# Optimization experiments

Hardware: AMD Instinct MI355X
Metric: run time of the kernel (lower is better)

Reference implementation:

```python
import jax, jax.numpy as jnp
import numpy as np

TOP_K = 2


def setup_inputs() -> dict:
    key = jax.random.key(0)
    ks = jax.random.split(key, 6)
    B, S, D, F, E = 4, 2048, 1024, 4096, 8
    sd = 1.0 / np.sqrt(D)
    sf = 1.0 / np.sqrt(F)
    return {
        "x": jax.random.normal(ks[0], (B, S, D), dtype=jnp.float32),
        "gate_w": jax.random.normal(ks[1], (D, E), dtype=jnp.float32) * sd,
        "w1": jax.random.normal(ks[2], (E, D, F), dtype=jnp.float32) * sd,
        "b1": jax.random.normal(ks[3], (E, F), dtype=jnp.float32) * 0.01,
        "w2": jax.random.normal(ks[4], (E, F, D), dtype=jnp.float32) * sf,
        "b2": jax.random.normal(ks[5], (E, D), dtype=jnp.float32) * 0.01,
    }


def reference(x, gate_w, w1, b1, w2, b2):
    B, S, D = x.shape
    E = gate_w.shape[1]
    xf = x.reshape(-1, D)                        # [T, D], T = B*S
    T = xf.shape[0]

    # Gating: top-k logits, softmax over the selected k (in fp32, as in torch)
    logits = xf @ gate_w                         # [T, E]
    top_vals, top_idx = jax.lax.top_k(logits, TOP_K)            # [T, K]
    wts = jax.nn.softmax(top_vals.astype(jnp.float32), axis=-1).astype(x.dtype)

    # Dense combine weights: combine[t, e] = sum_k wts[t,k] * [top_idx[t,k]==e]
    rows = jnp.arange(T)[:, None]
    combine = jnp.zeros((T, E), dtype=x.dtype).at[rows, top_idx].add(wts)

    # Expert FFNs (dropout is identity in eval; torch GELU default = exact erf)
    out = jnp.zeros_like(xf)
    for e in range(E):
        h = jax.nn.gelu(xf @ w1[e] + b1[e], approximate=False)  # [T, F]
        out = out + combine[:, e:e + 1] * (h @ w2[e] + b2[e])
    return out.reshape(B, S, D)
```

## Files before the change

### kernel.cpp

```cpp
#include <hip/hip_runtime.h>


#define T_TOK 8192
#define D_DIM 1024
#define F_DIM 4096
#define E_NUM 8
#define BM 256
#define BN 256
#define BK 64
#define NK1 (D_DIM / BK)
#define NK2 (F_DIM / BK)
#define NX1 (F_DIM / BN)
#define NX2 (D_DIM / BN)
#define MAX_TILES (T_TOK * 2 / BM + E_NUM)

typedef float f32x4 __attribute__((ext_vector_type(4)));
typedef short bf16x8 __attribute__((ext_vector_type(8)));

__device__ __forceinline__ unsigned short f2bf(float f) {
  union { float f; unsigned u; } v; v.f = f;
  unsigned r = v.u + 0x7FFFu + ((v.u >> 16) & 1u);
  return (unsigned short)(r >> 16);
}

__device__ __forceinline__ void async_cp16(const unsigned short* g, unsigned short* l) {
  __builtin_amdgcn_global_load_lds((__attribute__((address_space(1))) void*)g,
                                   (__attribute__((address_space(3))) void*)l,
                                   16, 0, 0);
}

#define WAIT_VM6 asm volatile("s_waitcnt vmcnt(6)" ::: "memory")
#define WAIT_LGKM0 asm volatile("s_waitcnt lgkmcnt(0)" ::: "memory")
#define RAW_BARRIER asm volatile("s_barrier" ::: "memory")


__global__ void cast_x_kernel(const float* __restrict__ src,
                              unsigned short* __restrict__ dst, int n4) {
  int i = blockIdx.x * blockDim.x + threadIdx.x;
  if (i >= n4) return;
  float4 v = ((const float4*)src)[i];
  ushort4 o;
  o.x = f2bf(v.x); o.y = f2bf(v.y); o.z = f2bf(v.z); o.w = f2bf(v.w);
  ((ushort4*)dst)[i] = o;
}

__global__ __launch_bounds__(256) void transpose_cast_kernel(
    const float* __restrict__ src, unsigned short* __restrict__ dst,
    int R, int C) {
  __shared__ float tile[64][65];
  int e = blockIdx.z;
  src += (size_t)e * R * C;
  dst += (size_t)e * R * C;
  int c0 = blockIdx.x * 64;
  int r0 = blockIdx.y * 64;
  int t = threadIdx.x;
  int cl = (t & 15) * 4, rl = t >> 4;
#pragma unroll
  for (int i = 0; i < 4; ++i) {
    int r = rl + i * 16;
    float4 v = *(const float4*)(src + (size_t)(r0 + r) * C + c0 + cl);
    tile[r][cl + 0] = v.x;
    tile[r][cl + 1] = v.y;
    tile[r][cl + 2] = v.z;
    tile[r][cl + 3] = v.w;
  }
  __syncthreads();
  int rl2 = (t & 15) * 4, cl2 = t >> 4;
#pragma unroll
  for (int i = 0; i < 4; ++i) {
    int c = cl2 + i * 16;
    ushort4 o;
    o.x = f2bf(tile[rl2 + 0][c]);
    o.y = f2bf(tile[rl2 + 1][c]);
    o.z = f2bf(tile[rl2 + 2][c]);
    o.w = f2bf(tile[rl2 + 3][c]);
    *(ushort4*)(dst + (size_t)(c0 + c) * R + r0 + rl2) = o;
  }
}

__global__ __launch_bounds__(256) void gate_kernel(
    const float* __restrict__ x, const float* __restrict__ gw,
    float* __restrict__ topk_w, int* __restrict__ topk_e) {
  int t = (blockIdx.x * 256 + threadIdx.x) >> 6;
  int lane = threadIdx.x & 63;
  const float* xr = x + (size_t)t * D_DIM;
  float acc[8];
#pragma unroll
  for (int e = 0; e < 8; ++e) acc[e] = 0.f;
  for (int j = 0; j < D_DIM / 64; ++j) {
    int d = lane + 64 * j;
    float xv = xr[d];
    float4 g0 = ((const float4*)(gw + (size_t)d * 8))[0];
    float4 g1 = ((const float4*)(gw + (size_t)d * 8))[1];
    acc[0] += xv * g0.x; acc[1] += xv * g0.y;
    acc[2] += xv * g0.z; acc[3] += xv * g0.w;
    acc[4] += xv * g1.x; acc[5] += xv * g1.y;
    acc[6] += xv * g1.z; acc[7] += xv * g1.w;
  }
#pragma unroll
  for (int off = 32; off > 0; off >>= 1) {
#pragma unroll
    for (int e = 0; e < 8; ++e) acc[e] += __shfl_xor(acc[e], off);
  }
  if (lane == 0) {
    int e0 = 0; float v0 = acc[0];
#pragma unroll
    for (int e = 1; e < 8; ++e)
      if (acc[e] > v0) { v0 = acc[e]; e0 = e; }
    int e1 = -1; float v1 = -1e30f;
#pragma unroll
    for (int e = 0; e < 8; ++e)
      if (e != e0 && acc[e] > v1) { v1 = acc[e]; e1 = e; }
    float ex = expf(v1 - v0);
    float inv = 1.f / (1.f + ex);
    topk_w[2 * t] = inv;
    topk_w[2 * t + 1] = ex * inv;
    topk_e[2 * t] = e0;
    topk_e[2 * t + 1] = e1;
  }
}

__global__ void scatter_kernel(const int* __restrict__ topk_e,
                               int* __restrict__ cnt, int* __restrict__ assign) {
  int idx = blockIdx.x * blockDim.x + threadIdx.x;
  int e = topk_e[idx];
  int pos = atomicAdd(&cnt[e], 1);
  assign[e * T_TOK + pos] = idx;
}

__global__ void tiles_kernel(const int* __restrict__ cnt,
                             int* __restrict__ ndesc, int4* __restrict__ desc) {
  if (threadIdx.x != 0) return;
  int nt = 0, hb = 0;
  for (int e = 0; e < E_NUM; ++e) {
    int c = cnt[e];
    for (int s = 0; s < c; s += BM) {
      int4 d;
      d.x = e; d.y = s; d.z = hb;
      d.w = (c - s < BM) ? (c - s) : BM;
      desc[nt++] = d;
    }
    hb += c;
  }
  *ndesc = nt;
}


__global__ __launch_bounds__(512, 2) void gemm1_kernel(
    const unsigned short* __restrict__ xb, const unsigned short* __restrict__ w1t,
    const float* __restrict__ b1, const int* __restrict__ assign,
    const int* __restrict__ ndesc, const int4* __restrict__ desc,
    unsigned short* __restrict__ H) {
  const int nwg = NX1 * MAX_TILES;
  int lin = blockIdx.y * NX1 + blockIdx.x;
  int wg = (lin & 7) * (nwg >> 3) + (lin >> 3);
  int tileid = wg / NX1;
  int n0 = (wg & (NX1 - 1)) * BN;
  if (tileid >= *ndesc) return;
  int4 dc = desc[tileid];
  int e = dc.x, start = dc.y, hbase = dc.z, mcnt = dc.w;

  extern __shared__ __attribute__((aligned(16))) unsigned short smem[];

  int tid = threadIdx.x, lane = tid & 63, wv = tid >> 6;

  int drow = tid >> 3, dcc = tid & 7;
  int g = (dcc - drow) & 7;
  const unsigned short* gAr[4];
  const unsigned short* gBr[4];
#pragma unroll
  for (int j = 0; j < 4; ++j) {
    int r = drow + 64 * j;
    int rc = r < mcnt ? r : (mcnt - 1);
    int a = assign[e * T_TOK + start + rc];
    gAr[j] = xb + (size_t)(a >> 1) * D_DIM + g * 8;
    gBr[j] = w1t + (size_t)(e * F_DIM + n0 + r) * D_DIM + g * 8;
  }
  int ldst = wv * 512;

  int kc16 = lane >> 4, r16 = lane & 15;
  int m_off = (wv & 1) * 128, n_off = (wv >> 1) * 64;

  f32x4 acc[8][4];
#pragma unroll
  for (int i = 0; i < 8; ++i)
#pragma unroll
    for (int j = 0; j < 4; ++j) acc[i][j] = (f32x4){0.f, 0.f, 0.f, 0.f};
  bf16x8 bfr[4][2];

  auto issueA = [&](int t, int j) {
    int kt = t < NK1 ? t : NK1 - 1;
    async_cp16(gAr[j] + kt * 64, smem + (t & 1) * 32768 + ldst + j * 4096);
  };
  auto issueB = [&](int t, int j) {
    int kt = t < NK1 ? t : NK1 - 1;
    async_cp16(gBr[j] + kt * 64, smem + (t & 1) * 32768 + 16384 + ldst + j * 4096);
  };

  auto phase = [&](int t, int q) {
    const unsigned short* Ab = smem + (t & 1) * 32768;
    const unsigned short* Bb = Ab + 16384;
    if (q == 0) {
#pragma unroll
      for (int j = 0; j < 4; ++j) {
        int rb = n_off + j * 16 + r16;
#pragma unroll
        for (int h = 0; h < 2; ++h)
          bfr[j][h] = *(const bf16x8*)(Bb + rb * 64 + ((h * 4 + kc16 + rb) & 7) * 8);
      }
    }
    bf16x8 af[2][2];
#pragma unroll
    for (int m2 = 0; m2 < 2; ++m2) {
      int ra = m_off + (2 * q + m2) * 16 + r16;
#pragma unroll
      for (int h = 0; h < 2; ++h)
        af[m2][h] = *(const bf16x8*)(Ab + ra * 64 + ((h * 4 + kc16 + ra) & 7) * 8);
    }
    if (q == 0)      { issueA(t + 1, 1); issueA(t + 1, 3); }
    else if (q == 1) { issueB(t + 2, 0); issueB(t + 2, 1); }
    else if (q == 2) { issueB(t + 2, 2); issueB(t + 2, 3); }
    else             { issueA(t + 2, 0); issueA(t + 2, 2); }
    RAW_BARRIER;
    WAIT_LGKM0;
    __builtin_amdgcn_s_setprio(1);
#pragma unroll
    for (int h = 0; h < 2; ++h)
#pragma unroll
      for (int m2 = 0; m2 < 2; ++m2)
#pragma unroll
        for (int j = 0; j < 4; ++j)
          acc[2 * q + m2][j] = __builtin_amdgcn_mfma_f32_16x16x32_bf16(
              af[m2][h], bfr[j][h], acc[2 * q + m2][j], 0, 0, 0);
    __builtin_amdgcn_s_setprio(0);
    if (q == 3) WAIT_VM6;
    RAW_BARRIER;
  };

#pragma unroll
  for (int j = 0; j < 4; ++j) issueB(0, j);
#pragma unroll
  for (int j = 0; j < 4; ++j) issueA(0, j);
  issueB(1, 0); issueB(1, 1); issueB(1, 2); issueB(1, 3);
  issueA(1, 0); issueA(1, 2);
  WAIT_VM6;
  RAW_BARRIER;

  for (int t = 0; t < NK1; ++t) {
    phase(t, 0); phase(t, 1); phase(t, 2); phase(t, 3);
  }

  int col = lane & 15, rbase = (lane >> 4) * 4;
  float bias[4];
#pragma unroll
  for (int j = 0; j < 4; ++j) bias[j] = b1[e * F_DIM + n0 + n_off + j * 16 + col];
#pragma unroll
  for (int i = 0; i < 8; ++i) {
#pragma unroll
    for (int rg = 0; rg < 4; ++rg) {
      int r = m_off + i * 16 + rbase + rg;
      if (r < mcnt) {
        unsigned short* hrow = H + (size_t)(hbase + start + r) * F_DIM + n0 + n_off + col;
#pragma unroll
        for (int j = 0; j < 4; ++j) {
          float v = acc[i][j][rg] + bias[j];
          v = 0.5f * v * (1.0f + erff(v * 0.70710678118654752f));
          hrow[j * 16] = f2bf(v);
        }
      }
    }
  }
}

__global__ __launch_bounds__(512, 2) void gemm2_kernel(
    const unsigned short* __restrict__ H, const unsigned short* __restrict__ w2t,
    const float* __restrict__ b2, const int* __restrict__ assign,
    const float* __restrict__ topk_w,
    const int* __restrict__ ndesc, const int4* __restrict__ desc,
    float* __restrict__ out) {
  const int nwg = NX2 * MAX_TILES;
  int lin = blockIdx.y * NX2 + blockIdx.x;
  int wg = (lin & 7) * (nwg >> 3) + (lin >> 3);
  int tileid = wg / NX2;
  int n0 = (wg & (NX2 - 1)) * BN;
  if (tileid >= *ndesc) return;
  int4 dc = desc[tileid];
  int e = dc.x, start = dc.y, hbase = dc.z, mcnt = dc.w;

  extern __shared__ __attribute__((aligned(16))) unsigned short smem[];

  int tid = threadIdx.x, lane = tid & 63, wv = tid >> 6;

  int drow = tid >> 3, dcc = tid & 7;
  int g = (dcc - drow) & 7;
  const unsigned short* gAr[4];
  const unsigned short* gBr[4];
#pragma unroll
  for (int j = 0; j < 4; ++j) {
    int r = drow + 64 * j;
    int rc = r < mcnt ? r : (mcnt - 1);
    gAr[j] = H + (size_t)(hbase + start + rc) * F_DIM + g * 8;
    gBr[j] = w2t + (size_t)(e * D_DIM + n0 + r) * F_DIM + g * 8;
  }
  int ldst = wv * 512;

  int kc16 = lane >> 4, r16 = lane & 15;
  int m_off = (wv & 1) * 128, n_off = (wv >> 1) * 64;

  f32x4 acc[8][4];
#pragma unroll
  for (int i = 0; i < 8; ++i)
#pragma unroll
    for (int j = 0; j < 4; ++j) acc[i][j] = (f32x4){0.f, 0.f, 0.f, 0.f};
  bf16x8 bfr[4][2];

  auto issueA = [&](int t, int j) {
    int kt = t < NK2 ? t : NK2 - 1;
    async_cp16(gAr[j] + kt * 64, smem + (t & 1) * 32768 + ldst + j * 4096);
  };
  auto issueB = [&](int t, int j) {
    int kt = t < NK2 ? t : NK2 - 1;
    async_cp16(gBr[j] + kt * 64, smem + (t & 1) * 32768 + 16384 + ldst + j * 4096);
  };

  auto phase = [&](int t, int q) {
    const unsigned short* Ab = smem + (t & 1) * 32768;
    const unsigned short* Bb = Ab + 16384;
    if (q == 0) {
#pragma unroll
      for (int j = 0; j < 4; ++j) {
        int rb = n_off + j * 16 + r16;
#pragma unroll
        for (int h = 0; h < 2; ++h)
          bfr[j][h] = *(const bf16x8*)(Bb + rb * 64 + ((h * 4 + kc16 + rb) & 7) * 8);
      }
    }
    bf16x8 af[2][2];
#pragma unroll
    for (int m2 = 0; m2 < 2; ++m2) {
      int ra = m_off + (2 * q + m2) * 16 + r16;
#pragma unroll
      for (int h = 0; h < 2; ++h)
        af[m2][h] = *(const bf16x8*)(Ab + ra * 64 + ((h * 4 + kc16 + ra) & 7) * 8);
    }
    if (q == 0)      { issueA(t + 1, 1); issueA(t + 1, 3); }
    else if (q == 1) { issueB(t + 2, 0); issueB(t + 2, 1); }
    else if (q == 2) { issueB(t + 2, 2); issueB(t + 2, 3); }
    else             { issueA(t + 2, 0); issueA(t + 2, 2); }
    RAW_BARRIER;
    WAIT_LGKM0;
    __builtin_amdgcn_s_setprio(1);
#pragma unroll
    for (int h = 0; h < 2; ++h)
#pragma unroll
      for (int m2 = 0; m2 < 2; ++m2)
#pragma unroll
        for (int j = 0; j < 4; ++j)
          acc[2 * q + m2][j] = __builtin_amdgcn_mfma_f32_16x16x32_bf16(
              af[m2][h], bfr[j][h], acc[2 * q + m2][j], 0, 0, 0);
    __builtin_amdgcn_s_setprio(0);
    if (q == 3) WAIT_VM6;
    RAW_BARRIER;
  };

#pragma unroll
  for (int j = 0; j < 4; ++j) issueB(0, j);
#pragma unroll
  for (int j = 0; j < 4; ++j) issueA(0, j);
  issueB(1, 0); issueB(1, 1); issueB(1, 2); issueB(1, 3);
  issueA(1, 0); issueA(1, 2);
  WAIT_VM6;
  RAW_BARRIER;

  for (int t = 0; t < NK2; ++t) {
    phase(t, 0); phase(t, 1); phase(t, 2); phase(t, 3);
  }

  int col = lane & 15, rbase = (lane >> 4) * 4;
  float bias[4];
#pragma unroll
  for (int j = 0; j < 4; ++j) bias[j] = b2[e * D_DIM + n0 + n_off + j * 16 + col];
#pragma unroll
  for (int i = 0; i < 8; ++i) {
#pragma unroll
    for (int rg = 0; rg < 4; ++rg) {
      int r = m_off + i * 16 + rbase + rg;
      if (r < mcnt) {
        int a = assign[e * T_TOK + start + r];
        float wt = topk_w[a];
        float* orow = out + (size_t)(a >> 1) * D_DIM + n0 + n_off + col;
#pragma unroll
        for (int j = 0; j < 4; ++j) {
          float v = acc[i][j][rg] + bias[j];
          atomicAdd(orow + j * 16, wt * v);
        }
      }
    }
  }
}


extern "C" void kernel_launch(void* const* d_in, const int* in_sizes, int n_in,
                              void* d_out, int out_size, void* d_ws, size_t ws_size,
                              hipStream_t stream) {
  const float* x      = (const float*)d_in[0];
  const float* gate_w = (const float*)d_in[1];
  const float* w1     = (const float*)d_in[2];
  const float* b1     = (const float*)d_in[3];
  const float* w2     = (const float*)d_in[4];
  const float* b2     = (const float*)d_in[5];
  float* out = (float*)d_out;

  char* ws = (char*)d_ws;
  size_t off = 0;
  auto alloc = [&](size_t bytes) {
    char* p = ws + off;
    off = (off + bytes + 255) & ~(size_t)255;
    return p;
  };
  unsigned short* xb   = (unsigned short*)alloc((size_t)T_TOK * D_DIM * 2);
  unsigned short* w1t  = (unsigned short*)alloc((size_t)E_NUM * D_DIM * F_DIM * 2);
  unsigned short* w2t  = (unsigned short*)alloc((size_t)E_NUM * D_DIM * F_DIM * 2);
  unsigned short* Hbuf = (unsigned short*)alloc((size_t)2 * T_TOK * F_DIM * 2);
  float* topk_w = (float*)alloc((size_t)2 * T_TOK * 4);
  int* topk_e   = (int*)alloc((size_t)2 * T_TOK * 4);
  int* assign   = (int*)alloc((size_t)E_NUM * T_TOK * 4);
  int* cnt      = (int*)alloc(64);
  int* ndesc    = (int*)alloc(64);
  int4* desc    = (int4*)alloc((size_t)MAX_TILES * 16);

  hipFuncSetAttribute(reinterpret_cast<const void*>(gemm1_kernel),
                      hipFuncAttributeMaxDynamicSharedMemorySize, 131072);
  hipFuncSetAttribute(reinterpret_cast<const void*>(gemm2_kernel),
                      hipFuncAttributeMaxDynamicSharedMemorySize, 131072);

  hipMemsetAsync(cnt, 0, 64, stream);
  hipMemsetAsync(out, 0, (size_t)out_size * 4, stream);

  cast_x_kernel<<<(T_TOK * D_DIM / 4 + 255) / 256, 256, 0, stream>>>(
      x, xb, T_TOK * D_DIM / 4);
  transpose_cast_kernel<<<dim3(F_DIM / 64, D_DIM / 64, E_NUM), 256, 0, stream>>>(
      w1, w1t, D_DIM, F_DIM);
  transpose_cast_kernel<<<dim3(D_DIM / 64, F_DIM / 64, E_NUM), 256, 0, stream>>>(
      w2, w2t, F_DIM, D_DIM);
  gate_kernel<<<T_TOK / 4, 256, 0, stream>>>(x, gate_w, topk_w, topk_e);
  scatter_kernel<<<2 * T_TOK / 256, 256, 0, stream>>>(topk_e, cnt, assign);
  tiles_kernel<<<1, 64, 0, stream>>>(cnt, ndesc, desc);
  gemm1_kernel<<<dim3(NX1, MAX_TILES), 512, 131072, stream>>>(
      xb, w1t, b1, assign, ndesc, desc, Hbuf);
  gemm2_kernel<<<dim3(NX2, MAX_TILES), 512, 131072, stream>>>(
      Hbuf, w2t, b2, assign, topk_w, ndesc, desc, out);
}
```

Before: 935.1 us.

## Shrink gemm2 M-tile, fuse x cast into gate, aggregate scatter atomics

The x-to-bf16 cast moves into the gate kernel, removing a separate pass. The transpose-cast kernel now writes wider 16-byte stores. Scatter uses wave-level ballot aggregation, so there is one atomic per expert per wave. gemm2 gets its own 128-row tile descriptors, with smaller LDS use and a two-phase pipeline to increase workgroup count and occupancy for the narrow N=1024 GEMM. One barrier is also dropped in gemm1's phase loop, which risks an LDS race if the remaining synchronization is insufficient.

```diff
diff --git a/kernel.cpp b/kernel.cpp
--- a/kernel.cpp
+++ b/kernel.cpp
@@ -13,9 +13,12 @@
 #define NX1 (F_DIM / BN)
 #define NX2 (D_DIM / BN)
 #define MAX_TILES (T_TOK * 2 / BM + E_NUM)
+#define BM2 128
+#define MAX_TILES2 (T_TOK * 2 / BM2 + E_NUM)
 
 typedef float f32x4 __attribute__((ext_vector_type(4)));
 typedef short bf16x8 __attribute__((ext_vector_type(8)));
+typedef unsigned short u16x8 __attribute__((ext_vector_type(8)));
 
 __device__ __forceinline__ unsigned short f2bf(float f) {
   union { float f; unsigned u; } v; v.f = f;
@@ -30,19 +33,10 @@
 }
 
 #define WAIT_VM6 asm volatile("s_waitcnt vmcnt(6)" ::: "memory")
+#define WAIT_VM4 asm volatile("s_waitcnt vmcnt(4)" ::: "memory")
 #define WAIT_LGKM0 asm volatile("s_waitcnt lgkmcnt(0)" ::: "memory")
 #define RAW_BARRIER asm volatile("s_barrier" ::: "memory")
 
-
-__global__ void cast_x_kernel(const float* __restrict__ src,
-                              unsigned short* __restrict__ dst, int n4) {
-  int i = blockIdx.x * blockDim.x + threadIdx.x;
-  if (i >= n4) return;
-  float4 v = ((const float4*)src)[i];
-  ushort4 o;
-  o.x = f2bf(v.x); o.y = f2bf(v.y); o.z = f2bf(v.z); o.w = f2bf(v.w);
-  ((ushort4*)dst)[i] = o;
-}
 
 __global__ __launch_bounds__(256) void transpose_cast_kernel(
     const float* __restrict__ src, unsigned short* __restrict__ dst,
@@ -65,31 +59,32 @@
     tile[r][cl + 3] = v.w;
   }
   __syncthreads();
-  int rl2 = (t & 15) * 4, cl2 = t >> 4;
-#pragma unroll
-  for (int i = 0; i < 4; ++i) {
-    int c = cl2 + i * 16;
-    ushort4 o;
-    o.x = f2bf(tile[rl2 + 0][c]);
-    o.y = f2bf(tile[rl2 + 1][c]);
-    o.z = f2bf(tile[rl2 + 2][c]);
-    o.w = f2bf(tile[rl2 + 3][c]);
-    *(ushort4*)(dst + (size_t)(c0 + c) * R + r0 + rl2) = o;
+  int rl2 = (t & 7) * 8, cl2 = t >> 3;
+#pragma unroll
+  for (int i = 0; i < 2; ++i) {
+    int c = cl2 + i * 32;
+    u16x8 o;
+#pragma unroll
+    for (int k = 0; k < 8; ++k) o[k] = f2bf(tile[rl2 + k][c]);
+    *(u16x8*)(dst + (size_t)(c0 + c) * R + r0 + rl2) = o;
   }
 }
 
 __global__ __launch_bounds__(256) void gate_kernel(
     const float* __restrict__ x, const float* __restrict__ gw,
-    float* __restrict__ topk_w, int* __restrict__ topk_e) {
+    float* __restrict__ topk_w, int* __restrict__ topk_e,
+    unsigned short* __restrict__ xb) {
   int t = (blockIdx.x * 256 + threadIdx.x) >> 6;
   int lane = threadIdx.x & 63;
   const float* xr = x + (size_t)t * D_DIM;
+  unsigned short* xbr = xb + (size_t)t * D_DIM;
   float acc[8];
 #pragma unroll
   for (int e = 0; e < 8; ++e) acc[e] = 0.f;
   for (int j = 0; j < D_DIM / 64; ++j) {
     int d = lane + 64 * j;
     float xv = xr[d];
+    xbr[d] = f2bf(xv);
     float4 g0 = ((const float4*)(gw + (size_t)d * 8))[0];
     float4 g1 = ((const float4*)(gw + (size_t)d * 8))[1];
     acc[0] += xv * g0.x; acc[1] += xv * g0.y;
@@ -124,14 +119,26 @@
                                int* __restrict__ cnt, int* __restrict__ assign) {
   int idx = blockIdx.x * blockDim.x + threadIdx.x;
   int e = topk_e[idx];
-  int pos = atomicAdd(&cnt[e], 1);
-  assign[e * T_TOK + pos] = idx;
+  int lane = threadIdx.x & 63;
+#pragma unroll
+  for (int ex = 0; ex < E_NUM; ++ex) {
+    unsigned long long m = __ballot(e == ex);
+    if (e == ex) {
+      int src = __ffsll((unsigned long long)m) - 1;
+      int nbefore = __popcll(m & ((1ull << lane) - 1ull));
+      int base = 0;
+      if (lane == src) base = atomicAdd(&cnt[ex], __popcll(m));
+      base = __shfl(base, src);
+      assign[ex * T_TOK + base + nbefore] = idx;
+    }
+  }
 }
 
 __global__ void tiles_kernel(const int* __restrict__ cnt,
-                             int* __restrict__ ndesc, int4* __restrict__ desc) {
+                             int* __restrict__ ndesc, int4* __restrict__ desc,
+                             int4* __restrict__ desc2) {
   if (threadIdx.x != 0) return;
-  int nt = 0, hb = 0;
+  int nt = 0, nt2 = 0, hb = 0;
   for (int e = 0; e < E_NUM; ++e) {
     int c = cnt[e];
     for (int s = 0; s < c; s += BM) {
@@ -140,9 +147,16 @@
       d.w = (c - s < BM) ? (c - s) : BM;
       desc[nt++] = d;
     }
+    for (int s = 0; s < c; s += BM2) {
+      int4 d;
+      d.x = e; d.y = s; d.z = hb;
+      d.w = (c - s < BM2) ? (c - s) : BM2;
+      desc2[nt2++] = d;
+    }
     hb += c;
   }
-  *ndesc = nt;
+  ndesc[0] = nt;
+  ndesc[1] = nt2;
 }
 
 
@@ -156,7 +170,7 @@
   int wg = (lin & 7) * (nwg >> 3) + (lin >> 3);
   int tileid = wg / NX1;
   int n0 = (wg & (NX1 - 1)) * BN;
-  if (tileid >= *ndesc) return;
+  if (tileid >= ndesc[0]) return;
   int4 dc = desc[tileid];
   int e = dc.x, start = dc.y, hbase = dc.z, mcnt = dc.w;
 
@@ -221,7 +235,6 @@
     else if (q == 1) { issueB(t + 2, 0); issueB(t + 2, 1); }
     else if (q == 2) { issueB(t + 2, 2); issueB(t + 2, 3); }
     else             { issueA(t + 2, 0); issueA(t + 2, 2); }
-    RAW_BARRIER;
     WAIT_LGKM0;
     __builtin_amdgcn_s_setprio(1);
 #pragma unroll
@@ -272,19 +285,20 @@
   }
 }
 
+
 __global__ __launch_bounds__(512, 2) void gemm2_kernel(
     const unsigned short* __restrict__ H, const unsigned short* __restrict__ w2t,
     const float* __restrict__ b2, const int* __restrict__ assign,
     const float* __restrict__ topk_w,
-    const int* __restrict__ ndesc, const int4* __restrict__ desc,
+    const int* __restrict__ ndesc, const int4* __restrict__ desc2,
     float* __restrict__ out) {
-  const int nwg = NX2 * MAX_TILES;
+  const int nwg = NX2 * MAX_TILES2;
   int lin = blockIdx.y * NX2 + blockIdx.x;
   int wg = (lin & 7) * (nwg >> 3) + (lin >> 3);
   int tileid = wg / NX2;
   int n0 = (wg & (NX2 - 1)) * BN;
-  if (tileid >= *ndesc) return;
-  int4 dc = desc[tileid];
+  if (tileid >= ndesc[1]) return;
+  int4 dc = desc2[tileid];
   int e = dc.x, start = dc.y, hbase = dc.z, mcnt = dc.w;
 
   extern __shared__ __attribute__((aligned(16))) unsigned short smem[];
@@ -293,39 +307,46 @@
 
   int drow = tid >> 3, dcc = tid & 7;
   int g = (dcc - drow) & 7;
-  const unsigned short* gAr[4];
-  const unsigned short* gBr[4];
+  const unsigned short* gA2[2];
+  const unsigned short* gB2[4];
+#pragma unroll
+  for (int j = 0; j < 2; ++j) {
+    int r = (drow & 31) + (drow >> 5) * 64 + j * 32;
+    int rc = r < mcnt ? r : (mcnt - 1);
+    gA2[j] = H + (size_t)(hbase + start + rc) * F_DIM + g * 8;
+  }
 #pragma unroll
   for (int j = 0; j < 4; ++j) {
-    int r = drow + 64 * j;
-    int rc = r < mcnt ? r : (mcnt - 1);
-    gAr[j] = H + (size_t)(hbase + start + rc) * F_DIM + g * 8;
-    gBr[j] = w2t + (size_t)(e * D_DIM + n0 + r) * F_DIM + g * 8;
-  }
-  int ldst = wv * 512;
+    int r = drow + j * 64;
+    gB2[j] = w2t + (size_t)(e * D_DIM + n0 + r) * F_DIM + g * 8;
+  }
+  int arowbase = ((wv * 8) & 31) + ((wv * 8) >> 5) * 64;
+  int ldstB = wv * 512;
 
   int kc16 = lane >> 4, r16 = lane & 15;
-  int m_off = (wv & 1) * 128, n_off = (wv >> 1) * 64;
-
-  f32x4 acc[8][4];
-#pragma unroll
-  for (int i = 0; i < 8; ++i)
+  int m_off = (wv & 1) * 64, n_off = (wv >> 1) * 64;
+
+  f32x4 acc[4][4];
+#pragma unroll
+  for (int i = 0; i < 4; ++i)
 #pragma unroll
     for (int j = 0; j < 4; ++j) acc[i][j] = (f32x4){0.f, 0.f, 0.f, 0.f};
   bf16x8 bfr[4][2];
 
   auto issueA = [&](int t, int j) {
     int kt = t < NK2 ? t : NK2 - 1;
-    async_cp16(gAr[j] + kt * 64, smem + (t & 1) * 32768 + ldst + j * 4096);
+    async_cp16(gA2[j] + kt * 64,
+               smem + (t & 1) * 24576 + (arowbase + j * 32) * 64);
   };
   auto issueB = [&](int t, int j) {
     int kt = t < NK2 ? t : NK2 - 1;
-    async_cp16(gBr[j] + kt * 64, smem + (t & 1) * 32768 + 16384 + ldst + j * 4096);
+    async_cp16(gB2[j] + kt * 64,
+               smem + (t & 1) * 24576 + 8192 + ldstB + j * 4096);
   };
 
   auto phase = [&](int t, int q) {
-    const unsigned short* Ab = smem + (t & 1) * 32768;
-    const unsigned short* Bb = Ab + 16384;
+    const unsigned short* Ab = smem + (t & 1) * 24576;
+    const unsigned short* Bb = Ab + 8192;
     if (q == 0) {
 #pragma unroll
       for (int j = 0; j < 4; ++j) {
@@ -343,11 +364,8 @@
       for (int h = 0; h < 2; ++h)
         af[m2][h] = *(const bf16x8*)(Ab + ra * 64 + ((h * 4 + kc16 + ra) & 7) * 8);
     }
-    if (q == 0)      { issueA(t + 1, 1); issueA(t + 1, 3); }
-    else if (q == 1) { issueB(t + 2, 0); issueB(t + 2, 1); }
-    else if (q == 2) { issueB(t + 2, 2); issueB(t + 2, 3); }
-    else             { issueA(t + 2, 0); issueA(t + 2, 2); }
-    RAW_BARRIER;
+    if (q == 0) { issueB(t + 1, 3); issueA(t + 1, 1); }
+    else        { issueB(t + 2, 0); issueB(t + 2, 1); issueB(t + 2, 2); issueA(t + 2, 0); }
     WAIT_LGKM0;
     __builtin_amdgcn_s_setprio(1);
 #pragma unroll
@@ -359,29 +377,25 @@
           acc[2 * q + m2][j] = __builtin_amdgcn_mfma_f32_16x16x32_bf16(
               af[m2][h], bfr[j][h], acc[2 * q + m2][j], 0, 0, 0);
     __builtin_amdgcn_s_setprio(0);
-    if (q == 3) WAIT_VM6;
+    if (q == 1) WAIT_VM4;
     RAW_BARRIER;
   };
 
-#pragma unroll
-  for (int j = 0; j < 4; ++j) issueB(0, j);
-#pragma unroll
-  for (int j = 0; j < 4; ++j) issueA(0, j);
-  issueB(1, 0); issueB(1, 1); issueB(1, 2); issueB(1, 3);
-  issueA(1, 0); issueA(1, 2);
-  WAIT_VM6;
+  issueB(0, 0); issueB(0, 1); issueB(0, 2); issueB(0, 3);
+  issueA(0, 0); issueA(0, 1);
+  issueB(1, 0); issueB(1, 1); issueB(1, 2);
+  issueA(1, 0);
+  WAIT_VM4;
   RAW_BARRIER;
 
-  for (int t = 0; t < NK2; ++t) {
-    phase(t, 0); phase(t, 1); phase(t, 2); phase(t, 3);
-  }
+  for (int t = 0; t < NK2; ++t) { phase(t, 0); phase(t, 1); }
 
   int col = lane & 15, rbase = (lane >> 4) * 4;
   float bias[4];
 #pragma unroll
   for (int j = 0; j < 4; ++j) bias[j] = b2[e * D_DIM + n0 + n_off + j * 16 + col];
 #pragma unroll
-  for (int i = 0; i < 8; ++i) {
+  for (int i = 0; i < 4; ++i) {
 #pragma unroll
     for (int rg = 0; rg < 4; ++rg) {
       int r = m_off + i * 16 + rbase + rg;
@@ -428,26 +442,25 @@
   int* cnt      = (int*)alloc(64);
   int* ndesc    = (int*)alloc(64);
   int4* desc    = (int4*)alloc((size_t)MAX_TILES * 16);
+  int4* desc2   = (int4*)alloc((size_t)MAX_TILES2 * 16);
 
   hipFuncSetAttribute(reinterpret_cast<const void*>(gemm1_kernel),
                       hipFuncAttributeMaxDynamicSharedMemorySize, 131072);
   hipFuncSetAttribute(reinterpret_cast<const void*>(gemm2_kernel),
-                      hipFuncAttributeMaxDynamicSharedMemorySize, 131072);
+                      hipFuncAttributeMaxDynamicSharedMemorySize, 98304);
 
   hipMemsetAsync(cnt, 0, 64, stream);
   hipMemsetAsync(out, 0, (size_t)out_size * 4, stream);
 
-  cast_x_kernel<<<(T_TOK * D_DIM / 4 + 255) / 256, 256, 0, stream>>>(
-      x, xb, T_TOK * D_DIM / 4);
   transpose_cast_kernel<<<dim3(F_DIM / 64, D_DIM / 64, E_NUM), 256, 0, stream>>>(
       w1, w1t, D_DIM, F_DIM);
   transpose_cast_kernel<<<dim3(D_DIM / 64, F_DIM / 64, E_NUM), 256, 0, stream>>>(
       w2, w2t, F_DIM, D_DIM);
-  gate_kernel<<<T_TOK / 4, 256, 0, stream>>>(x, gate_w, topk_w, topk_e);
+  gate_kernel<<<T_TOK / 4, 256, 0, stream>>>(x, gate_w, topk_w, topk_e, xb);
   scatter_kernel<<<2 * T_TOK / 256, 256, 0, stream>>>(topk_e, cnt, assign);
-  tiles_kernel<<<1, 64, 0, stream>>>(cnt, ndesc, desc);
+  tiles_kernel<<<1, 64, 0, stream>>>(cnt, ndesc, desc, desc2);
   gemm1_kernel<<<dim3(NX1, MAX_TILES), 512, 131072, stream>>>(
       xb, w1t, b1, assign, ndesc, desc, Hbuf);
-  gemm2_kernel<<<dim3(NX2, MAX_TILES), 512, 131072, stream>>>(
-      Hbuf, w2t, b2, assign, topk_w, ndesc, desc, out);
-}
+  gemm2_kernel<<<dim3(NX2, MAX_TILES2), 512, 98304, stream>>>(
+      Hbuf, w2t, b2, assign, topk_w, ndesc, desc2, out);
+}
```

New measurement: 860.9 us. 7.9% less time.
